# Performance work log

Hardware: AMD Instinct MI355X
Metric: run time of the kernel (lower is better)

Reference implementation:

```python
import jax, jax.numpy as jnp
import numpy as np

B, N, C = 8, 2048, 512  # batch, points, channels; dk == C


def _mlp(x, W, b):
    # torch MLP helper = Linear followed by ReLU (even on the last layer)
    return jax.nn.relu(x @ W + b)


def setup_inputs() -> dict:
    key = jax.random.key(0)
    ks = jax.random.split(key, 5)
    s = 1.0 / np.sqrt(C)
    return {
        "x": jax.random.normal(ks[0], (B, N, C), dtype=jnp.float32),
        "Wh": jax.random.normal(ks[1], (C, C), dtype=jnp.float32) * s,
        "bh": jnp.zeros((C,), dtype=jnp.float32),
        "Wl": jax.random.normal(ks[2], (C, C), dtype=jnp.float32) * s,
        "bl": jnp.zeros((C,), dtype=jnp.float32),
        "Wg": jax.random.normal(ks[3], (C, C), dtype=jnp.float32) * s,
        "bg": jnp.zeros((C,), dtype=jnp.float32),
        "Wm": jax.random.normal(ks[4], (C, C), dtype=jnp.float32) * s,
        "bm": jnp.zeros((C,), dtype=jnp.float32),
    }


def reference(x, Wh, bh, Wl, bl, Wg, bg, Wm, bm):
    h = _mlp(x, Wh, bh)                      # [B, N, dk] (torch transposes; folded into einsum)
    l = _mlp(x, Wl, bl)                      # [B, N, dk]
    scores = jnp.einsum("bnd,bmd->bnm", l, h)  # [B, N, N]
    attn = jax.nn.softmax(scores, axis=-1)
    g = _mlp(x, Wg, bg)                      # [B, N, C]
    out = x + jnp.einsum("bnm,bmc->bnc", attn, g)
    return _mlp(out, Wm, bm)
```

## Files before the change

kernel.cpp:

```cpp
#include <hip/hip_runtime.h>


typedef __attribute__((ext_vector_type(4))) float f32x4;
typedef __attribute__((ext_vector_type(8))) short s16x8;
typedef __attribute__((ext_vector_type(4))) short s16x4;
typedef __attribute__((ext_vector_type(8))) _Float16 f16x8;
typedef __attribute__((ext_vector_type(4))) unsigned u32x4;

typedef unsigned int u32;
typedef __attribute__((address_space(1))) const u32 gu32;
typedef __attribute__((address_space(3))) u32 lu32;

__device__ __forceinline__ void gload16(const short* g, short* l) {
  __builtin_amdgcn_global_load_lds((gu32*)g, (lu32*)l, 16, 0, 0);
}

__device__ __forceinline__ short f2h(float f) {
  _Float16 h = (_Float16)f;
  return __builtin_bit_cast(short, h);
}

__device__ __forceinline__ unsigned pk2h(float a, float b) {
  return __builtin_bit_cast(unsigned, __builtin_amdgcn_cvt_pkrtz(a, b));
}

#define MFMA(a, b, c) __builtin_amdgcn_mfma_f32_16x16x32_f16(a, b, c, 0, 0, 0)


__global__ __launch_bounds__(256) void conv_x_kernel(const float* __restrict__ x,
                                                     short* __restrict__ xb) {
  int i = blockIdx.x * 256 + threadIdx.x;
  const float4* xv = (const float4*)x;
  float4 a = xv[2 * i], b = xv[2 * i + 1];
  s16x8 o;
  o[0] = f2h(a.x); o[1] = f2h(a.y); o[2] = f2h(a.z); o[3] = f2h(a.w);
  o[4] = f2h(b.x); o[5] = f2h(b.y); o[6] = f2h(b.z); o[7] = f2h(b.w);
  ((s16x8*)xb)[i] = o;
}

__global__ __launch_bounds__(256) void conv_w_kernel(const float* __restrict__ Wh,
                                                     const float* __restrict__ Wl,
                                                     const float* __restrict__ Wg,
                                                     const float* __restrict__ Wm,
                                                     short* __restrict__ Wt) {
  int idx = blockIdx.x * 256 + threadIdx.x;
  int k = idx & 511, n = (idx >> 9) & 511, w = idx >> 18;
  const float* W = (w == 0) ? Wh : (w == 1) ? Wl : (w == 2) ? Wg : Wm;
  Wt[idx] = f2h(W[k * 512 + n]);
}


__global__ __launch_bounds__(256) void mlp3_kernel(const short* __restrict__ A,
                                                   const short* __restrict__ Wt_all,
                                                   const float* __restrict__ bh,
                                                   const float* __restrict__ bl,
                                                   const float* __restrict__ bg,
                                                   short* __restrict__ h,
                                                   short* __restrict__ l,
                                                   short* __restrict__ gT) {
  int z = blockIdx.z;
  const short* Wt = Wt_all + z * 262144;
  const float* bias = (z == 0) ? bh : (z == 1) ? bl : bg;

  __shared__ __align__(16) short lds_a[128 * 40];
  __shared__ __align__(16) short lds_b[128 * 40];
  int tid = threadIdx.x, lane = tid & 63, w = tid >> 6;
  int wm = w >> 1, wn = w & 1;
  int bm = blockIdx.x * 128, bn = blockIdx.y * 128;

  f32x4 acc[4][4];
#pragma unroll
  for (int mi = 0; mi < 4; ++mi)
#pragma unroll
    for (int ni = 0; ni < 4; ++ni) acc[mi][ni] = (f32x4){0.f, 0.f, 0.f, 0.f};

  for (int k0 = 0; k0 < 512; k0 += 32) {
#pragma unroll
    for (int it = 0; it < 2; ++it) {
      int chunk = tid + it * 256;
      int row = chunk >> 2, c8 = (chunk & 3) * 8;
      *(s16x8*)&lds_a[row * 40 + c8] =
          *(const s16x8*)&A[(size_t)(bm + row) * 512 + k0 + c8];
      *(s16x8*)&lds_b[row * 40 + c8] =
          *(const s16x8*)&Wt[(bn + row) * 512 + k0 + c8];
    }
    __syncthreads();
    f16x8 af[4], bfr[4];
#pragma unroll
    for (int mi = 0; mi < 4; ++mi)
      af[mi] = *(const f16x8*)&lds_a[(wm * 64 + mi * 16 + (lane & 15)) * 40 +
                                     (lane >> 4) * 8];
#pragma unroll
    for (int ni = 0; ni < 4; ++ni)
      bfr[ni] = *(const f16x8*)&lds_b[(wn * 64 + ni * 16 + (lane & 15)) * 40 +
                                      (lane >> 4) * 8];
#pragma unroll
    for (int mi = 0; mi < 4; ++mi)
#pragma unroll
      for (int ni = 0; ni < 4; ++ni) acc[mi][ni] = MFMA(af[mi], bfr[ni], acc[mi][ni]);
    __syncthreads();
  }

#pragma unroll
  for (int mi = 0; mi < 4; ++mi)
#pragma unroll
    for (int ni = 0; ni < 4; ++ni) {
      int col = bn + wn * 64 + ni * 16 + (lane & 15);
      float bv = bias[col];
#pragma unroll
      for (int r = 0; r < 4; ++r) {
        int row = bm + wm * 64 + mi * 16 + (lane >> 4) * 4 + r;
        float v = fmaxf(acc[mi][ni][r] + bv, 0.0f);
        short o = f2h(v);
        if (z == 0) h[(size_t)row * 512 + col] = o;
        else if (z == 1) l[(size_t)row * 512 + col] = o;
        else {
          int bb = row >> 11, mm = row & 2047;
          gT[((size_t)bb * 512 + col) * 2048 + mm] = o;
        }
      }
    }
}


__global__ __launch_bounds__(256, 1) void attn_kernel(const short* __restrict__ lmat,
                                                      const short* __restrict__ hmat,
                                                      const short* __restrict__ gT,
                                                      const float* __restrict__ x,
                                                      short* __restrict__ y) {
  __shared__ __align__(16) short kbuf[2][16384];
  __shared__ __align__(16) short gbuf[2][16384];
  int tid = threadIdx.x, lane = tid & 63, w = tid >> 6;
  int swz = (blockIdx.x & 7) * 32 + (blockIdx.x >> 3);
  int b = swz >> 5, qt = swz & 31;
  int q0 = qt * 64 + w * 16;
  const short* lb = lmat + (size_t)b * 2048 * 512;
  const short* hb = hmat + (size_t)b * 2048 * 512;
  const short* gb = gT + (size_t)b * 512 * 2048;

  int r0 = lane & 15, g = lane >> 4;

  f16x8 qf[16];
  {
    int q = q0 + r0;
#pragma unroll
    for (int ks = 0; ks < 16; ++ks)
      qf[ks] = *(const f16x8*)&lb[(size_t)q * 512 + ks * 32 + g * 8];
  }
  f32x4 accO[32];
#pragma unroll
  for (int i = 0; i < 32; ++i) accO[i] = (f32x4){0.f, 0.f, 0.f, 0.f};
  float mrun = -3e38f, lsumL = 0.f;

  auto stageK = [&](int buf, int t) {
    int key0 = t * 32;
    short* kd = &kbuf[buf][0];
#pragma unroll
    for (int j = 0; j < 8; ++j) {
      int wl = w * 8 + j;
      gload16(hb + (size_t)(key0 + wl) * 512 + (((lane * 16) ^ ((wl & 7) << 4)) >> 1),
              kd + wl * 512);
    }
  };
  auto stageG = [&](int buf, int t) {
    int key0 = t * 32;
    short* gd = &gbuf[buf][0];
#pragma unroll
    for (int j = 0; j < 8; ++j) {
      int wl = w * 8 + j;
      int c = wl * 16 + (lane >> 2);
      gload16(gb + (size_t)c * 2048 + key0 + (lane & 3) * 8, gd + wl * 512);
    }
  };
  auto QK = [&](int buf, f32x4& o0, f32x4& o1) {
    const short* kb = &kbuf[buf][0];
#pragma unroll
    for (int ks = 0; ks < 16; ++ks) {
      f16x8 k0f = *(const f16x8*)&kb[(r0 * 512 + ks * 32 + g * 8) ^ ((r0 & 7) << 3)];
      o0 = MFMA(k0f, qf[ks], o0);
      f16x8 k1f = *(const f16x8*)&kb[((r0 + 16) * 512 + ks * 32 + g * 8) ^ ((r0 & 7) << 3)];
      o1 = MFMA(k1f, qf[ks], o1);
    }
  };

  stageK(0, 0); stageG(0, 0); stageK(1, 1);
  __syncthreads();
  f32x4 sc0 = {0.f, 0.f, 0.f, 0.f}, sc1 = {0.f, 0.f, 0.f, 0.f};
  f32x4 sn0, sn1;
  QK(0, sc0, sc1);
  __syncthreads();

  for (int t = 0; t < 64; ++t) {
    if (t < 62) stageK(t & 1, t + 2);
    if (t < 63) stageG((t + 1) & 1, t + 1);

    sn0 = (f32x4){0.f, 0.f, 0.f, 0.f};
    sn1 = (f32x4){0.f, 0.f, 0.f, 0.f};
    if (t < 63) {
      __builtin_amdgcn_s_setprio(1);
      QK((t + 1) & 1, sn0, sn1);
      __builtin_amdgcn_s_setprio(0);
    }

    float m2 = fmaxf(fmaxf(fmaxf(sc0[0], sc0[1]), fmaxf(sc0[2], sc0[3])),
                     fmaxf(fmaxf(sc1[0], sc1[1]), fmaxf(sc1[2], sc1[3])));
    m2 = fmaxf(m2, __shfl_xor(m2, 16));
    m2 = fmaxf(m2, __shfl_xor(m2, 32));
    bool ok = (m2 <= mrun + 8.0f);
    if (!__all((int)ok)) {
      float mnew = fmaxf(mrun, m2);
      float s = __expf(mrun - mnew);
      mrun = mnew;
      lsumL *= s;
#pragma unroll
      for (int nf = 0; nf < 32; ++nf) accO[nf] *= s;
    }
    float a0 = __expf(sc0[0] - mrun), a1 = __expf(sc0[1] - mrun);
    float a2 = __expf(sc0[2] - mrun), a3 = __expf(sc0[3] - mrun);
    float b0 = __expf(sc1[0] - mrun), b1 = __expf(sc1[1] - mrun);
    float b2 = __expf(sc1[2] - mrun), b3 = __expf(sc1[3] - mrun);
    lsumL += (a0 + a1) + (a2 + a3) + (b0 + b1) + (b2 + b3);

    unsigned A0 = pk2h(a0, a1), A1 = pk2h(a2, a3);
    unsigned B0 = pk2h(b0, b1), B1 = pk2h(b2, b3);
    asm volatile("v_permlane32_swap_b32 %0, %1" : "+v"(A0), "+v"(B0));
    asm volatile("v_permlane16_swap_b32 %0, %1" : "+v"(A0), "+v"(B0));
    asm volatile("v_permlane32_swap_b32 %0, %1" : "+v"(A1), "+v"(B1));
    asm volatile("v_permlane16_swap_b32 %0, %1" : "+v"(A1), "+v"(B1));
    u32x4 pw = {A0, A1, B0, B1};
    f16x8 pfrag = __builtin_bit_cast(f16x8, pw);

    const short* gp = &gbuf[t & 1][0];
    __builtin_amdgcn_s_setprio(1);
#pragma unroll
    for (int nf = 0; nf < 32; ++nf) {
      f16x8 gf = *(const f16x8*)&gp[(nf * 16 + r0) * 32 + g * 8];
      accO[nf] = MFMA(gf, pfrag, accO[nf]);
    }
    __builtin_amdgcn_s_setprio(0);

    __syncthreads();
    sc0 = sn0; sc1 = sn1;
  }

  float ls = lsumL;
  ls += __shfl_xor(ls, 16);
  ls += __shfl_xor(ls, 32);
  float inv = 1.0f / ls;
  int q = q0 + r0;
#pragma unroll
  for (int nf = 0; nf < 32; ++nf) {
    int d0 = nf * 16 + g * 4;
    float4 xr = *(const float4*)&x[((size_t)b * 2048 + q) * 512 + d0];
    s16x4 o;
    o[0] = f2h(accO[nf][0] * inv + xr.x);
    o[1] = f2h(accO[nf][1] * inv + xr.y);
    o[2] = f2h(accO[nf][2] * inv + xr.z);
    o[3] = f2h(accO[nf][3] * inv + xr.w);
    *(s16x4*)&y[((size_t)b * 2048 + q) * 512 + d0] = o;
  }
}


__global__ __launch_bounds__(256) void final_gemm_kernel(const short* __restrict__ A,
                                                         const short* __restrict__ Wt,
                                                         const float* __restrict__ bias,
                                                         float* __restrict__ out) {
  __shared__ __align__(16) short lds_a[128 * 40];
  __shared__ __align__(16) short lds_b[128 * 40];
  int tid = threadIdx.x, lane = tid & 63, w = tid >> 6;
  int wm = w >> 1, wn = w & 1;
  int bm = blockIdx.x * 128, bn = blockIdx.y * 128;

  f32x4 acc[4][4];
#pragma unroll
  for (int mi = 0; mi < 4; ++mi)
#pragma unroll
    for (int ni = 0; ni < 4; ++ni) acc[mi][ni] = (f32x4){0.f, 0.f, 0.f, 0.f};

  for (int k0 = 0; k0 < 512; k0 += 32) {
#pragma unroll
    for (int it = 0; it < 2; ++it) {
      int chunk = tid + it * 256;
      int row = chunk >> 2, c8 = (chunk & 3) * 8;
      *(s16x8*)&lds_a[row * 40 + c8] =
          *(const s16x8*)&A[(size_t)(bm + row) * 512 + k0 + c8];
      *(s16x8*)&lds_b[row * 40 + c8] =
          *(const s16x8*)&Wt[(bn + row) * 512 + k0 + c8];
    }
    __syncthreads();
    f16x8 af[4], bfr[4];
#pragma unroll
    for (int mi = 0; mi < 4; ++mi)
      af[mi] = *(const f16x8*)&lds_a[(wm * 64 + mi * 16 + (lane & 15)) * 40 +
                                     (lane >> 4) * 8];
#pragma unroll
    for (int ni = 0; ni < 4; ++ni)
      bfr[ni] = *(const f16x8*)&lds_b[(wn * 64 + ni * 16 + (lane & 15)) * 40 +
                                      (lane >> 4) * 8];
#pragma unroll
    for (int mi = 0; mi < 4; ++mi)
#pragma unroll
      for (int ni = 0; ni < 4; ++ni) acc[mi][ni] = MFMA(af[mi], bfr[ni], acc[mi][ni]);
    __syncthreads();
  }

#pragma unroll
  for (int mi = 0; mi < 4; ++mi)
#pragma unroll
    for (int ni = 0; ni < 4; ++ni) {
      int col = bn + wn * 64 + ni * 16 + (lane & 15);
      float bv = bias[col];
#pragma unroll
      for (int r = 0; r < 4; ++r) {
        int row = bm + wm * 64 + mi * 16 + (lane >> 4) * 4 + r;
        out[(size_t)row * 512 + col] = fmaxf(acc[mi][ni][r] + bv, 0.0f);
      }
    }
}


extern "C" void kernel_launch(void* const* d_in, const int* in_sizes, int n_in,
                              void* d_out, int out_size, void* d_ws, size_t ws_size,
                              hipStream_t stream) {
  const float* x  = (const float*)d_in[0];
  const float* Wh = (const float*)d_in[1];
  const float* bh = (const float*)d_in[2];
  const float* Wl = (const float*)d_in[3];
  const float* bl = (const float*)d_in[4];
  const float* Wg = (const float*)d_in[5];
  const float* bg = (const float*)d_in[6];
  const float* Wm = (const float*)d_in[7];
  const float* bm = (const float*)d_in[8];

  char* ws = (char*)d_ws;
  const size_t SZ = 16777216;
  short* xb  = (short*)(ws + 0 * SZ);
  short* h   = (short*)(ws + 1 * SZ);
  short* l   = (short*)(ws + 2 * SZ);
  short* gT  = (short*)(ws + 3 * SZ);
  short* y   = (short*)(ws + 4 * SZ);
  short* Wt  = (short*)(ws + 5 * SZ);

  conv_x_kernel<<<4096, 256, 0, stream>>>(x, xb);
  conv_w_kernel<<<4096, 256, 0, stream>>>(Wh, Wl, Wg, Wm, Wt);
  mlp3_kernel<<<dim3(128, 4, 3), 256, 0, stream>>>(xb, Wt, bh, bl, bg, h, l, gT);
  attn_kernel<<<256, 256, 0, stream>>>(l, h, gT, x, y);
  final_gemm_kernel<<<dim3(128, 4), 256, 0, stream>>>(y, Wt + 3 * 262144, bm,
                                                      (float*)d_out);
}
```

Before: 286.9 us.

## Pad G tile in LDS and stage it through registers to avoid bank conflicts

The G tile is now loaded into registers with ordinary global loads and written to LDS with a padded row stride of 40 halves, replacing direct global-to-LDS loads into an unpadded 32-wide layout. The padding is meant to remove LDS bank conflicts on the 16-byte fragment reads in the PV MFMA loop. In exchange it uses 8 extra vector registers per thread and more LDS. The LDS write now happens after the MFMA loop, so the global load latency must be hidden by the QK and softmax work in between.

```diff
diff --git a/kernel.cpp b/kernel.cpp
--- a/kernel.cpp
+++ b/kernel.cpp
@@ -123,13 +123,15 @@
 }
 
 
+#define GSTR 40
+
 __global__ __launch_bounds__(256, 1) void attn_kernel(const short* __restrict__ lmat,
                                                       const short* __restrict__ hmat,
                                                       const short* __restrict__ gT,
                                                       const float* __restrict__ x,
                                                       short* __restrict__ y) {
   __shared__ __align__(16) short kbuf[2][16384];
-  __shared__ __align__(16) short gbuf[2][16384];
+  __shared__ __align__(16) short gbuf[2][512 * GSTR];
   int tid = threadIdx.x, lane = tid & 63, w = tid >> 6;
   int swz = (blockIdx.x & 7) * 32 + (blockIdx.x >> 3);
   int b = swz >> 5, qt = swz & 31;
@@ -152,6 +154,21 @@
   for (int i = 0; i < 32; ++i) accO[i] = (f32x4){0.f, 0.f, 0.f, 0.f};
   float mrun = -3e38f, lsumL = 0.f;
 
+  s16x8 greg[8];
+  int gc = (w * 8) * 16 + (lane >> 2);
+  int gk = (lane & 3) * 8;
+
+  auto loadG = [&](int t) {
+    int key0 = t * 32;
+#pragma unroll
+    for (int j = 0; j < 8; ++j)
+      greg[j] = *(const s16x8*)&gb[(size_t)(gc + j * 16) * 2048 + key0 + gk];
+  };
+  auto writeG = [&](int buf) {
+#pragma unroll
+    for (int j = 0; j < 8; ++j)
+      *(s16x8*)&gbuf[buf][(gc + j * 16) * GSTR + gk] = greg[j];
+  };
   auto stageK = [&](int buf, int t) {
     int key0 = t * 32;
     short* kd = &kbuf[buf][0];
@@ -160,16 +177,6 @@
       int wl = w * 8 + j;
       gload16(hb + (size_t)(key0 + wl) * 512 + (((lane * 16) ^ ((wl & 7) << 4)) >> 1),
               kd + wl * 512);
-    }
-  };
-  auto stageG = [&](int buf, int t) {
-    int key0 = t * 32;
-    short* gd = &gbuf[buf][0];
-#pragma unroll
-    for (int j = 0; j < 8; ++j) {
-      int wl = w * 8 + j;
-      int c = wl * 16 + (lane >> 2);
-      gload16(gb + (size_t)c * 2048 + key0 + (lane & 3) * 8, gd + wl * 512);
     }
   };
   auto QK = [&](int buf, f32x4& o0, f32x4& o1) {
@@ -183,7 +190,10 @@
     }
   };
 
-  stageK(0, 0); stageG(0, 0); stageK(1, 1);
+  loadG(0);
+  stageK(0, 0);
+  stageK(1, 1);
+  writeG(0);
   __syncthreads();
   f32x4 sc0 = {0.f, 0.f, 0.f, 0.f}, sc1 = {0.f, 0.f, 0.f, 0.f};
   f32x4 sn0, sn1;
@@ -191,8 +201,8 @@
   __syncthreads();
 
   for (int t = 0; t < 64; ++t) {
+    if (t < 63) loadG(t + 1);
     if (t < 62) stageK(t & 1, t + 2);
-    if (t < 63) stageG((t + 1) & 1, t + 1);
 
     sn0 = (f32x4){0.f, 0.f, 0.f, 0.f};
     sn1 = (f32x4){0.f, 0.f, 0.f, 0.f};
@@ -234,10 +244,12 @@
     __builtin_amdgcn_s_setprio(1);
 #pragma unroll
     for (int nf = 0; nf < 32; ++nf) {
-      f16x8 gf = *(const f16x8*)&gp[(nf * 16 + r0) * 32 + g * 8];
+      f16x8 gf = *(const f16x8*)&gp[(nf * 16 + r0) * GSTR + g * 8];
       accO[nf] = MFMA(gf, pfrag, accO[nf]);
     }
     __builtin_amdgcn_s_setprio(0);
+
+    if (t < 63) writeG((t + 1) & 1);
 
     __syncthreads();
     sc0 = sn0; sc1 = sn1;
```

New measurement: 296.4 us. 1.03x slower.

## Split attention keys across two blocks and merge partials in a combine kernel

Applied to the files above, without the earlier changes.

The attention kernel now splits each query tile's 2048 keys into two halves handled by separate blocks. Each block writes unnormalized fp16 partial outputs plus its running max and sum, and a new combine kernel merges the two halves and adds the residual x. Key tiles shrink to 16, LDS use is halved and launch bounds allow two blocks per CU, doubling resident waves to hide latency better. The costs are an extra kernel launch, extra global traffic for the partials and fp32 x, and use of the narrower 16x16x16 MFMA in the PV product.

```diff
diff --git a/kernel.cpp b/kernel.cpp
--- a/kernel.cpp
+++ b/kernel.cpp
@@ -5,7 +5,8 @@
 typedef __attribute__((ext_vector_type(8))) short s16x8;
 typedef __attribute__((ext_vector_type(4))) short s16x4;
 typedef __attribute__((ext_vector_type(8))) _Float16 f16x8;
-typedef __attribute__((ext_vector_type(4))) unsigned u32x4;
+typedef __attribute__((ext_vector_type(4))) _Float16 f16x4;
+typedef __attribute__((ext_vector_type(2))) unsigned u32x2;
 
 typedef unsigned int u32;
 typedef __attribute__((address_space(1))) const u32 gu32;
@@ -25,6 +26,7 @@
 }
 
 #define MFMA(a, b, c) __builtin_amdgcn_mfma_f32_16x16x32_f16(a, b, c, 0, 0, 0)
+#define MFMA16(a, b, c) __builtin_amdgcn_mfma_f32_16x16x16f16(a, b, c, 0, 0, 0)
 
 
 __global__ __launch_bounds__(256) void conv_x_kernel(const float* __restrict__ x,
@@ -123,20 +125,24 @@
 }
 
 
-__global__ __launch_bounds__(256, 1) void attn_kernel(const short* __restrict__ lmat,
-                                                      const short* __restrict__ hmat,
-                                                      const short* __restrict__ gT,
-                                                      const float* __restrict__ x,
-                                                      short* __restrict__ y) {
-  __shared__ __align__(16) short kbuf[2][16384];
-  __shared__ __align__(16) short gbuf[2][16384];
+__global__ __launch_bounds__(256, 2) void attn_split_kernel(
+    const short* __restrict__ lmat, const short* __restrict__ hmat,
+    const short* __restrict__ gT,
+    short* __restrict__ OA, short* __restrict__ OB,
+    float2* __restrict__ mlA, float2* __restrict__ mlB) {
+  __shared__ __align__(16) short kbuf[2][8192];
+  __shared__ __align__(16) short gbuf[2][8192];
   int tid = threadIdx.x, lane = tid & 63, w = tid >> 6;
-  int swz = (blockIdx.x & 7) * 32 + (blockIdx.x >> 3);
-  int b = swz >> 5, qt = swz & 31;
+  int b = blockIdx.x & 7;
+  int idx = blockIdx.x >> 3;
+  int qt = idx >> 1, sp = idx & 1;
   int q0 = qt * 64 + w * 16;
+  int keybase = sp * 1024;
   const short* lb = lmat + (size_t)b * 2048 * 512;
   const short* hb = hmat + (size_t)b * 2048 * 512;
   const short* gb = gT + (size_t)b * 512 * 2048;
+  short* Op = sp ? OB : OA;
+  float2* ml = sp ? mlB : mlA;
 
   int r0 = lane & 15, g = lane >> 4;
 
@@ -153,57 +159,52 @@
   float mrun = -3e38f, lsumL = 0.f;
 
   auto stageK = [&](int buf, int t) {
-    int key0 = t * 32;
+    int key0 = keybase + t * 16;
     short* kd = &kbuf[buf][0];
 #pragma unroll
-    for (int j = 0; j < 8; ++j) {
-      int wl = w * 8 + j;
+    for (int j = 0; j < 4; ++j) {
+      int wl = w * 4 + j;
       gload16(hb + (size_t)(key0 + wl) * 512 + (((lane * 16) ^ ((wl & 7) << 4)) >> 1),
               kd + wl * 512);
     }
   };
   auto stageG = [&](int buf, int t) {
-    int key0 = t * 32;
+    int key0 = keybase + t * 16;
     short* gd = &gbuf[buf][0];
 #pragma unroll
-    for (int j = 0; j < 8; ++j) {
-      int wl = w * 8 + j;
-      int c = wl * 16 + (lane >> 2);
-      gload16(gb + (size_t)c * 2048 + key0 + (lane & 3) * 8, gd + wl * 512);
+    for (int j = 0; j < 4; ++j) {
+      int wl = w * 4 + j;
+      int row = wl * 32 + (lane >> 1);
+      gload16(gb + (size_t)row * 2048 + key0 + (lane & 1) * 8, gd + wl * 512);
     }
   };
-  auto QK = [&](int buf, f32x4& o0, f32x4& o1) {
+  auto QK = [&](int buf, f32x4& o) {
     const short* kb = &kbuf[buf][0];
 #pragma unroll
     for (int ks = 0; ks < 16; ++ks) {
-      f16x8 k0f = *(const f16x8*)&kb[(r0 * 512 + ks * 32 + g * 8) ^ ((r0 & 7) << 3)];
-      o0 = MFMA(k0f, qf[ks], o0);
-      f16x8 k1f = *(const f16x8*)&kb[((r0 + 16) * 512 + ks * 32 + g * 8) ^ ((r0 & 7) << 3)];
-      o1 = MFMA(k1f, qf[ks], o1);
+      f16x8 kf = *(const f16x8*)&kb[(r0 * 512 + ks * 32 + g * 8) ^ ((r0 & 7) << 3)];
+      o = MFMA(kf, qf[ks], o);
     }
   };
 
   stageK(0, 0); stageG(0, 0); stageK(1, 1);
   __syncthreads();
-  f32x4 sc0 = {0.f, 0.f, 0.f, 0.f}, sc1 = {0.f, 0.f, 0.f, 0.f};
-  f32x4 sn0, sn1;
-  QK(0, sc0, sc1);
+  f32x4 sc = {0.f, 0.f, 0.f, 0.f};
+  QK(0, sc);
   __syncthreads();
 
   for (int t = 0; t < 64; ++t) {
     if (t < 62) stageK(t & 1, t + 2);
     if (t < 63) stageG((t + 1) & 1, t + 1);
 
-    sn0 = (f32x4){0.f, 0.f, 0.f, 0.f};
-    sn1 = (f32x4){0.f, 0.f, 0.f, 0.f};
+    f32x4 sn = {0.f, 0.f, 0.f, 0.f};
     if (t < 63) {
       __builtin_amdgcn_s_setprio(1);
-      QK((t + 1) & 1, sn0, sn1);
+      QK((t + 1) & 1, sn);
       __builtin_amdgcn_s_setprio(0);
     }
 
-    float m2 = fmaxf(fmaxf(fmaxf(sc0[0], sc0[1]), fmaxf(sc0[2], sc0[3])),
-                     fmaxf(fmaxf(sc1[0], sc1[1]), fmaxf(sc1[2], sc1[3])));
+    float m2 = fmaxf(fmaxf(sc[0], sc[1]), fmaxf(sc[2], sc[3]));
     m2 = fmaxf(m2, __shfl_xor(m2, 16));
     m2 = fmaxf(m2, __shfl_xor(m2, 32));
     bool ok = (m2 <= mrun + 8.0f);
@@ -215,32 +216,24 @@
 #pragma unroll
       for (int nf = 0; nf < 32; ++nf) accO[nf] *= s;
     }
-    float a0 = __expf(sc0[0] - mrun), a1 = __expf(sc0[1] - mrun);
-    float a2 = __expf(sc0[2] - mrun), a3 = __expf(sc0[3] - mrun);
-    float b0 = __expf(sc1[0] - mrun), b1 = __expf(sc1[1] - mrun);
-    float b2 = __expf(sc1[2] - mrun), b3 = __expf(sc1[3] - mrun);
-    lsumL += (a0 + a1) + (a2 + a3) + (b0 + b1) + (b2 + b3);
-
-    unsigned A0 = pk2h(a0, a1), A1 = pk2h(a2, a3);
-    unsigned B0 = pk2h(b0, b1), B1 = pk2h(b2, b3);
-    asm volatile("v_permlane32_swap_b32 %0, %1" : "+v"(A0), "+v"(B0));
-    asm volatile("v_permlane16_swap_b32 %0, %1" : "+v"(A0), "+v"(B0));
-    asm volatile("v_permlane32_swap_b32 %0, %1" : "+v"(A1), "+v"(B1));
-    asm volatile("v_permlane16_swap_b32 %0, %1" : "+v"(A1), "+v"(B1));
-    u32x4 pw = {A0, A1, B0, B1};
-    f16x8 pfrag = __builtin_bit_cast(f16x8, pw);
+    float p0 = __expf(sc[0] - mrun), p1 = __expf(sc[1] - mrun);
+    float p2 = __expf(sc[2] - mrun), p3 = __expf(sc[3] - mrun);
+    lsumL += (p0 + p1) + (p2 + p3);
+
+    u32x2 pw = {pk2h(p0, p1), pk2h(p2, p3)};
+    f16x4 pfrag = __builtin_bit_cast(f16x4, pw);
 
     const short* gp = &gbuf[t & 1][0];
     __builtin_amdgcn_s_setprio(1);
 #pragma unroll
     for (int nf = 0; nf < 32; ++nf) {
-      f16x8 gf = *(const f16x8*)&gp[(nf * 16 + r0) * 32 + g * 8];
-      accO[nf] = MFMA(gf, pfrag, accO[nf]);
+      f16x4 gf = *(const f16x4*)&gp[(nf * 16 + r0) * 16 + g * 4];
+      accO[nf] = MFMA16(gf, pfrag, accO[nf]);
     }
     __builtin_amdgcn_s_setprio(0);
 
     __syncthreads();
-    sc0 = sn0; sc1 = sn1;
+    sc = sn;
   }
 
   float ls = lsumL;
@@ -250,15 +243,42 @@
   int q = q0 + r0;
 #pragma unroll
   for (int nf = 0; nf < 32; ++nf) {
-    int d0 = nf * 16 + g * 4;
-    float4 xr = *(const float4*)&x[((size_t)b * 2048 + q) * 512 + d0];
     s16x4 o;
-    o[0] = f2h(accO[nf][0] * inv + xr.x);
-    o[1] = f2h(accO[nf][1] * inv + xr.y);
-    o[2] = f2h(accO[nf][2] * inv + xr.z);
-    o[3] = f2h(accO[nf][3] * inv + xr.w);
-    *(s16x4*)&y[((size_t)b * 2048 + q) * 512 + d0] = o;
-  }
+    o[0] = f2h(accO[nf][0] * inv);
+    o[1] = f2h(accO[nf][1] * inv);
+    o[2] = f2h(accO[nf][2] * inv);
+    o[3] = f2h(accO[nf][3] * inv);
+    *(s16x4*)&Op[((size_t)b * 2048 + q) * 512 + nf * 16 + g * 4] = o;
+  }
+  if (g == 0) ml[(size_t)b * 2048 + q] = make_float2(mrun, ls);
+}
+
+
+__global__ __launch_bounds__(256) void combine_kernel(
+    const short* __restrict__ OA, const short* __restrict__ OB,
+    const float2* __restrict__ mlA, const float2* __restrict__ mlB,
+    const float* __restrict__ x, short* __restrict__ y) {
+  int i = blockIdx.x * 256 + threadIdx.x;
+  int base = i * 8, q = i >> 6;
+  float2 a = mlA[q], c = mlB[q];
+  float ms = fmaxf(a.x, c.x);
+  float wA = __expf(a.x - ms) * a.y;
+  float wB = __expf(c.x - ms) * c.y;
+  float inv = 1.0f / (wA + wB);
+  f16x8 oa = *(const f16x8*)&OA[base];
+  f16x8 ob = *(const f16x8*)&OB[base];
+  float4 x0 = *(const float4*)&x[base];
+  float4 x1 = *(const float4*)&x[base + 4];
+  s16x8 o;
+  o[0] = f2h(((float)oa[0] * wA + (float)ob[0] * wB) * inv + x0.x);
+  o[1] = f2h(((float)oa[1] * wA + (float)ob[1] * wB) * inv + x0.y);
+  o[2] = f2h(((float)oa[2] * wA + (float)ob[2] * wB) * inv + x0.z);
+  o[3] = f2h(((float)oa[3] * wA + (float)ob[3] * wB) * inv + x0.w);
+  o[4] = f2h(((float)oa[4] * wA + (float)ob[4] * wB) * inv + x1.x);
+  o[5] = f2h(((float)oa[5] * wA + (float)ob[5] * wB) * inv + x1.y);
+  o[6] = f2h(((float)oa[6] * wA + (float)ob[6] * wB) * inv + x1.z);
+  o[7] = f2h(((float)oa[7] * wA + (float)ob[7] * wB) * inv + x1.w);
+  *(s16x8*)&y[base] = o;
 }
 
 
@@ -335,17 +355,20 @@
 
   char* ws = (char*)d_ws;
   const size_t SZ = 16777216;
-  short* xb  = (short*)(ws + 0 * SZ);
-  short* h   = (short*)(ws + 1 * SZ);
-  short* l   = (short*)(ws + 2 * SZ);
-  short* gT  = (short*)(ws + 3 * SZ);
-  short* y   = (short*)(ws + 4 * SZ);
-  short* Wt  = (short*)(ws + 5 * SZ);
+  short*  xb  = (short*)(ws + 0 * SZ);
+  short*  h   = (short*)(ws + 1 * SZ);
+  short*  l   = (short*)(ws + 2 * SZ);
+  short*  gT  = (short*)(ws + 3 * SZ);
+  short*  yOB = (short*)(ws + 4 * SZ);
+  short*  Wt  = (short*)(ws + 5 * SZ);
+  float2* mlA = (float2*)(ws + 5 * SZ + 2097152);
+  float2* mlB = (float2*)(ws + 5 * SZ + 2097152 + 131072);
 
   conv_x_kernel<<<4096, 256, 0, stream>>>(x, xb);
   conv_w_kernel<<<4096, 256, 0, stream>>>(Wh, Wl, Wg, Wm, Wt);
   mlp3_kernel<<<dim3(128, 4, 3), 256, 0, stream>>>(xb, Wt, bh, bl, bg, h, l, gT);
-  attn_kernel<<<256, 256, 0, stream>>>(l, h, gT, x, y);
-  final_gemm_kernel<<<dim3(128, 4), 256, 0, stream>>>(y, Wt + 3 * 262144, bm,
+  attn_split_kernel<<<512, 256, 0, stream>>>(l, h, gT, xb, yOB, mlA, mlB);
+  combine_kernel<<<4096, 256, 0, stream>>>(xb, yOB, mlA, mlB, x, yOB);
+  final_gemm_kernel<<<dim3(128, 4), 256, 0, stream>>>(yOB, Wt + 3 * 262144, bm,
                                                       (float*)d_out);
 }
```

Measured after the change: 293.0 us. 2.1% more time.
